# Performance work log

Hardware: AMD Instinct MI355X
Metric: run time of the kernel (lower is better)

Reference implementation:

```python
import jax, jax.numpy as jnp
import numpy as np

D_MODEL = 1024
D_STATE = 16
D_CONV = 4
D_INNER = 2 * D_MODEL          # expand * d_model
DT_RANK = (D_MODEL + 15) // 16 # ceil(d_model/16) = 64
BATCH, SEQLEN = 2, 1024


def setup_inputs() -> dict:
    key = jax.random.key(0)
    ks = jax.random.split(key, 8)
    s = lambda k, shape, scale=0.02: (jax.random.normal(k, shape, jnp.float32) * scale)
    return {
        "hidden_states": jax.random.normal(ks[0], (BATCH, SEQLEN, D_MODEL), jnp.float32),
        "in_proj_w": s(ks[1], (2 * D_INNER, D_MODEL)),
        "conv_w": s(ks[2], (D_INNER, 1, D_CONV), 0.3),   # depthwise conv kernel (O, I/groups=1, K)
        "conv_b": jnp.zeros((D_INNER,), jnp.float32),
        "x_proj_w": s(ks[3], (DT_RANK + 2 * D_STATE, D_INNER)),
        "dt_proj_w": s(ks[4], (D_INNER, DT_RANK), 0.1),
        # inverse-softplus of small dt values, like the torch init
        "dt_proj_b": jax.random.uniform(ks[5], (D_INNER,), jnp.float32, minval=-5.0, maxval=-2.0),
        "A_log": jnp.log(jnp.broadcast_to(jnp.arange(1, D_STATE + 1, dtype=jnp.float32), (D_INNER, D_STATE))),
        "D": jnp.ones((D_INNER,), jnp.float32),
        "out_proj_w": s(ks[6], (D_MODEL, D_INNER)),
    }


def _forward(hidden_states, in_proj_w, conv_w, conv_b, x_proj_w,
             dt_proj_w, dt_proj_b, A_log, D, out_proj_w):
    B, L, _ = hidden_states.shape
    # in_proj -> split into x, z
    xz = hidden_states @ in_proj_w.T                      # [B, L, 2*d_inner]
    x, z = jnp.split(xz, 2, axis=-1)
    # causal depthwise conv1d (pad left d_conv-1, then take first L) + SiLU
    xc = jnp.transpose(x, (0, 2, 1))                      # [B, d_inner, L]
    xc = jax.lax.conv_general_dilated(
        xc, conv_w, window_strides=(1,), padding=[(D_CONV - 1, 0)],
        feature_group_count=D_INNER,
        dimension_numbers=("NCH", "OIH", "NCH")) + conv_b[None, :, None]
    xc = jax.nn.silu(xc)
    u = jnp.transpose(xc, (0, 2, 1)).astype(jnp.float32)  # [B, L, d_inner]
    # x_proj -> dt_low, B, C
    x_dbl = u @ x_proj_w.T                                # [B, L, dt_rank + 2*d_state]
    dt_low, Bp, Cp = jnp.split(x_dbl, [DT_RANK, DT_RANK + D_STATE], axis=-1)
    dt = dt_low @ dt_proj_w.T + dt_proj_b                 # [B, L, d_inner]
    # NOTE: original adds dt_proj.bias AGAIN as delta_bias inside the scan, then softplus
    delta = jax.nn.softplus(dt + dt_proj_b)
    A = -jnp.exp(A_log.astype(jnp.float32))               # [d_inner, d_state]
    # discretization
    dA = jnp.exp(jnp.einsum("bld,dn->lbdn", delta, A))    # [L, B, d, n]
    dBu = jnp.einsum("bld,bln,bld->lbdn", delta, Bp.astype(jnp.float32), u)
    C_t = jnp.transpose(Cp.astype(jnp.float32), (1, 0, 2))  # [L, B, n]

    def step(state, inp):
        a, b, c = inp
        state = a * state + b                             # [B, d, n]
        y = jnp.einsum("bdn,bn->bd", state, c)
        return state, y

    x0 = jnp.zeros((B, D_INNER, D_STATE), jnp.float32)
    _, ys = jax.lax.scan(step, x0, (dA, dBu, C_t))        # ys: [L, B, d]
    y = jnp.transpose(ys, (1, 0, 2))                      # [B, L, d]
    y = y + u * D.astype(jnp.float32)                     # skip connection
    y = y * jax.nn.silu(z.astype(jnp.float32))            # gating
    y = y.astype(hidden_states.dtype)
    return y @ out_proj_w.T                               # [B, L, d_model]


def reference(hidden_states, in_proj_w, conv_w, conv_b, x_proj_w,
              dt_proj_w, dt_proj_b, A_log, D, out_proj_w):
    return _forward(hidden_states, in_proj_w, conv_w, conv_b, x_proj_w,
                    dt_proj_w, dt_proj_b, A_log, D, out_proj_w)
```

## Files before the change

kernel.cpp:

```cpp
#include <hip/hip_runtime.h>
#include <hip/hip_bf16.h>
#include <math.h>

#define BATCH   2
#define SEQLEN  1024
#define DMODEL  1024
#define DINNER  2048
#define DSTATE  16
#define DTRANK  64
#define XPAD    128
#define MROWS   (BATCH*SEQLEN)
#define NSEG2   32
#define SEGL2   (SEQLEN/NSEG2)
#define XP_SPLIT  8
#define OUT_SPLIT 2

typedef float    f32x4  __attribute__((ext_vector_type(4)));
typedef _Float16 f16x8  __attribute__((ext_vector_type(8)));
typedef _Float16 f16x4  __attribute__((ext_vector_type(4)));

template<int EPI>
__global__ __launch_bounds__(256) void pgemm64(
    const _Float16* __restrict__ A, int lda,
    const _Float16* __restrict__ W, int ldw,
    float* __restrict__ C, int ldc, int K,
    const float* __restrict__ bias, _Float16* __restrict__ C16, size_t zstride)
{
  constexpr int APS = 520;
  constexpr int BPS = 1032;
  __shared__ _Float16 As[2][8 * APS];
  __shared__ _Float16 Bs[2][8 * BPS];

  const int t  = threadIdx.x;
  const int m0 = blockIdx.y * 64, n0 = blockIdx.x * 128;
  const int kchunk = K / gridDim.z;
  const int kbeg = blockIdx.z * kchunk;
  const int nIter = kchunk / 64;

  const int kb = t & 7;
  const int r0 = t >> 3;
  const _Float16* gA = A + (size_t)(m0 + r0) * lda + kbeg + kb * 8;
  const _Float16* gB = W + (size_t)(n0 + r0) * ldw + kbeg + kb * 8;
  const size_t a32 = (size_t)32 * lda;
  const size_t b32 = (size_t)32 * ldw;
  const int aoff = kb * APS + r0 * 8;
  const int boff = kb * BPS + r0 * 8;

  {
    f16x8 a0 = *(const f16x8*)(gA);
    f16x8 a1 = *(const f16x8*)(gA + a32);
    f16x8 b0 = *(const f16x8*)(gB);
    f16x8 b1 = *(const f16x8*)(gB + b32);
    f16x8 b2 = *(const f16x8*)(gB + 2 * b32);
    f16x8 b3 = *(const f16x8*)(gB + 3 * b32);
    gA += 64; gB += 64;
    *(f16x8*)&As[0][aoff]       = a0;
    *(f16x8*)&As[0][aoff + 256] = a1;
    *(f16x8*)&Bs[0][boff]       = b0;
    *(f16x8*)&Bs[0][boff + 256] = b1;
    *(f16x8*)&Bs[0][boff + 512] = b2;
    *(f16x8*)&Bs[0][boff + 768] = b3;
  }

  const int lane = t & 63, wvi = t >> 6;
  const int wn = wvi * 32;
  const int lm = lane & 15, lk = lane >> 4;

  f32x4 acc[4][2] = {};

  for (int it = 0; it < nIter; ++it) {
    __syncthreads();
    const bool more = (it + 1 < nIter);
    f16x8 a0, a1, b0, b1, b2, b3;
    if (more) {
      a0 = *(const f16x8*)(gA);
      a1 = *(const f16x8*)(gA + a32);
      b0 = *(const f16x8*)(gB);
      b1 = *(const f16x8*)(gB + b32);
      b2 = *(const f16x8*)(gB + 2 * b32);
      b3 = *(const f16x8*)(gB + 3 * b32);
      gA += 64; gB += 64;
    }
    const int cb = it & 1;
#pragma unroll
    for (int s = 0; s < 2; ++s) {
      f16x8 av[4], bv[2];
#pragma unroll
      for (int i = 0; i < 4; ++i)
        av[i] = *(const f16x8*)&As[cb][(s * 4 + lk) * APS + (i * 16 + lm) * 8];
#pragma unroll
      for (int j = 0; j < 2; ++j)
        bv[j] = *(const f16x8*)&Bs[cb][(s * 4 + lk) * BPS + (wn + j * 16 + lm) * 8];
#pragma unroll
      for (int i = 0; i < 4; ++i)
#pragma unroll
        for (int j = 0; j < 2; ++j)
          acc[i][j] = __builtin_amdgcn_mfma_f32_16x16x32_f16(av[i], bv[j], acc[i][j], 0, 0, 0);
    }
    if (more) {
      const int nb = (it + 1) & 1;
      *(f16x8*)&As[nb][aoff]       = a0;
      *(f16x8*)&As[nb][aoff + 256] = a1;
      *(f16x8*)&Bs[nb][boff]       = b0;
      *(f16x8*)&Bs[nb][boff + 256] = b1;
      *(f16x8*)&Bs[nb][boff + 512] = b2;
      *(f16x8*)&Bs[nb][boff + 768] = b3;
    }
  }

  float* Cz = C + (size_t)blockIdx.z * zstride;
#pragma unroll
  for (int i = 0; i < 4; ++i) {
    const int mrow = m0 + i * 16 + lk * 4;
#pragma unroll
    for (int j = 0; j < 2; ++j) {
      const int col = n0 + wn + j * 16 + lm;
#pragma unroll
      for (int r = 0; r < 4; ++r)
        Cz[(size_t)(mrow + r) * ldc + col] = acc[i][j][r];
    }
  }
}

template<int EPI>
__global__ __launch_bounds__(256) void pgemm128(
    const _Float16* __restrict__ A, int lda,
    const _Float16* __restrict__ W, int ldw,
    float* __restrict__ C, int ldc, int K,
    _Float16* __restrict__ C16, size_t zstride)
{
  constexpr int PS = 1032;
  __shared__ _Float16 As[2][8 * PS];
  __shared__ _Float16 Bs[2][8 * PS];

  const int t  = threadIdx.x;
  const int m0 = blockIdx.y * 128, n0 = blockIdx.x * 128;
  const int kchunk = K / gridDim.z;
  const int kbeg = blockIdx.z * kchunk;
  const int nIter = kchunk / 64;

  const int kb = t & 7;
  const int r0 = t >> 3;
  const _Float16* gA = A + (size_t)(m0 + r0) * lda + kbeg + kb * 8;
  const _Float16* gB = W + (size_t)(n0 + r0) * ldw + kbeg + kb * 8;
  const size_t a32 = (size_t)32 * lda;
  const size_t b32 = (size_t)32 * ldw;
  const int soff = kb * PS + r0 * 8;

  {
    f16x8 ar[4], br[4];
#pragma unroll
    for (int j = 0; j < 4; ++j) {
      ar[j] = *(const f16x8*)(gA + j * a32);
      br[j] = *(const f16x8*)(gB + j * b32);
    }
    gA += 64; gB += 64;
#pragma unroll
    for (int j = 0; j < 4; ++j) {
      *(f16x8*)&As[0][soff + j * 256] = ar[j];
      *(f16x8*)&Bs[0][soff + j * 256] = br[j];
    }
  }

  const int lane = t & 63, wvi = t >> 6;
  const int wm = (wvi >> 1) * 64, wn = (wvi & 1) * 64;
  const int lm = lane & 15, lk = lane >> 4;

  f32x4 acc[4][4] = {};

  for (int it = 0; it < nIter; ++it) {
    __syncthreads();
    const bool more = (it + 1 < nIter);
    f16x8 ar[4], br[4];
    if (more) {
#pragma unroll
      for (int j = 0; j < 4; ++j) {
        ar[j] = *(const f16x8*)(gA + j * a32);
        br[j] = *(const f16x8*)(gB + j * b32);
      }
      gA += 64; gB += 64;
    }
    const int cb = it & 1;
#pragma unroll
    for (int s = 0; s < 2; ++s) {
      f16x8 av[4], bv[4];
#pragma unroll
      for (int i = 0; i < 4; ++i)
        av[i] = *(const f16x8*)&As[cb][(s * 4 + lk) * PS + (wm + i * 16 + lm) * 8];
#pragma unroll
      for (int j = 0; j < 4; ++j)
        bv[j] = *(const f16x8*)&Bs[cb][(s * 4 + lk) * PS + (wn + j * 16 + lm) * 8];
#pragma unroll
      for (int i = 0; i < 4; ++i)
#pragma unroll
        for (int j = 0; j < 4; ++j)
          acc[i][j] = __builtin_amdgcn_mfma_f32_16x16x32_f16(av[i], bv[j], acc[i][j], 0, 0, 0);
    }
    if (more) {
      const int nb = (it + 1) & 1;
#pragma unroll
      for (int j = 0; j < 4; ++j) {
        *(f16x8*)&As[nb][soff + j * 256] = ar[j];
        *(f16x8*)&Bs[nb][soff + j * 256] = br[j];
      }
    }
  }

  float* Cz = C + (size_t)blockIdx.z * zstride;
#pragma unroll
  for (int i = 0; i < 4; ++i) {
    const int mrow = m0 + wm + i * 16 + lk * 4;
#pragma unroll
    for (int j = 0; j < 4; ++j) {
      const int col = n0 + wn + j * 16 + lm;
#pragma unroll
      for (int r = 0; r < 4; ++r) {
        float v = acc[i][j][r];
        size_t off = (size_t)(mrow + r) * ldc + col;
        if constexpr (EPI == 0) {
          Cz[off] = v;
        } else {
          C16[off] = (_Float16)v;
        }
      }
    }
  }
}

#define R0 (MROWS * DMODEL / 4)
#define R1 (2 * DINNER * DMODEL / 4)
#define R2 (DMODEL * DINNER / 4)
#define R4 (XPAD * DINNER / 4)
#define F2H_TOTAL (R0 + R1 + R2 + R4)

__global__ __launch_bounds__(256) void f2h_all(
    const float* __restrict__ hid, const float* __restrict__ w_in,
    const float* __restrict__ w_out, const float* __restrict__ w_xp,
    _Float16* __restrict__ hid16, _Float16* __restrict__ w_in16,
    _Float16* __restrict__ w_out16, _Float16* __restrict__ w_xp16)
{
  int i = blockIdx.x * 256 + threadIdx.x;
  const float* src; _Float16* dst; int off;
  if (i < R0)                     { src = hid;   dst = hid16;   off = i; }
  else if (i < R0+R1)             { src = w_in;  dst = w_in16;  off = i - R0; }
  else if (i < R0+R1+R2)          { src = w_out; dst = w_out16; off = i - (R0+R1); }
  else if (i < F2H_TOTAL) {
    off = i - (R0+R1+R2);
    int r = (off * 4) >> 11;
    f16x4 h = {0, 0, 0, 0};
    if (r < 96) {
      float4 v = ((const float4*)w_xp)[off];
      h = (f16x4){(_Float16)v.x, (_Float16)v.y, (_Float16)v.z, (_Float16)v.w};
    }
    ((f16x4*)w_xp16)[off] = h;
    return;
  } else return;
  float4 v = ((const float4*)src)[off];
  ((f16x4*)dst)[off] = (f16x4){(_Float16)v.x, (_Float16)v.y, (_Float16)v.z, (_Float16)v.w};
}

__global__ __launch_bounds__(256) void reduce_xdbl(
    const float* __restrict__ part,
    float* __restrict__ xdbl32)
{
  int i = blockIdx.x * 256 + threadIdx.x;
  f32x4 s = ((const f32x4*)part)[i];
#pragma unroll
  for (int z = 1; z < XP_SPLIT; ++z)
    s += ((const f32x4*)part)[(size_t)z * (MROWS * XPAD / 4) + i];
  ((f32x4*)xdbl32)[i] = s;
}

__global__ __launch_bounds__(256) void reduce_out(
    const float* __restrict__ part, float* __restrict__ out)
{
  int i = blockIdx.x * 256 + threadIdx.x;
  f32x4 s = ((const f32x4*)part)[i];
#pragma unroll
  for (int z = 1; z < OUT_SPLIT; ++z)
    s += ((const f32x4*)part)[(size_t)z * (MROWS * DMODEL / 4) + i];
  ((f32x4*)out)[i] = s;
}

__global__ __launch_bounds__(256) void conv_silu(
    const _Float16* __restrict__ xz16,
    const float* __restrict__ conv_w,
    const float* __restrict__ conv_b,
    _Float16* __restrict__ u16)
{
  const int idx = blockIdx.x * 256 + threadIdx.x;
  const int d   = idx & (DINNER - 1);
  const int row = idx >> 11;
  const int l   = row & (SEQLEN - 1);
  float s = conv_b[d];
#pragma unroll
  for (int k = 0; k < 4; ++k) {
    int lt = l + k - 3;
    if (lt >= 0)
      s = fmaf((float)xz16[(size_t)(row + k - 3) * (2 * DINNER) + d],
               conv_w[d * 4 + k], s);
  }
  float v = s / (1.f + __expf(-s));
  u16[idx] = (_Float16)v;
}

__global__ __launch_bounds__(256) void scan_pe(
    const _Float16* __restrict__ u16,
    const float* __restrict__ x_dbl,
    const float* __restrict__ A_log,
    const float* __restrict__ dt_w,
    const float* __restrict__ dt_b,
    float* __restrict__ pbuf, float* __restrict__ ebuf,
    _Float16* __restrict__ delta16)
{
  const int t = threadIdx.x;
  const int d = blockIdx.x * 256 + t;
  const int b   = blockIdx.y >> 5;
  const int seg = blockIdx.y & 31;
  const int row0 = b * SEQLEN + seg * SEGL2;

  f32x4 w[16];
#pragma unroll
  for (int q = 0; q < 16; ++q)
    w[q] = *(const f32x4*)&dt_w[(size_t)d * DTRANK + q * 4];
  const float b2 = 2.f * dt_b[d];

  float A_dn[DSTATE];
#pragma unroll
  for (int q = 0; q < 4; ++q) {
    f32x4 a4 = *(const f32x4*)&A_log[(size_t)d * DSTATE + q * 4];
#pragma unroll
    for (int e = 0; e < 4; ++e) A_dn[q * 4 + e] = -__expf(a4[e]);
  }

  __shared__ __align__(16) float xd[SEGL2 * 64];
  __shared__ __align__(16) float Bl[SEGL2 * DSTATE];
  {
#pragma unroll
    for (int k = 0; k < 2; ++k) {
      int idx = t * 2 + k;
      int i = idx >> 4, c4 = (idx & 15) * 4;
      *(f32x4*)&xd[i * 64 + c4] =
          *(const f32x4*)&x_dbl[(size_t)(row0 + i) * XPAD + c4];
    }
    if (t < 128) {
      int i = t >> 2, n4 = (t & 3) * 4;
      *(f32x4*)&Bl[i * DSTATE + n4] =
          *(const f32x4*)&x_dbl[(size_t)(row0 + i) * XPAD + DTRANK + n4];
    }
  }
  __syncthreads();

  float E[DSTATE];
#pragma unroll
  for (int n = 0; n < DSTATE; ++n) E[n] = 0.f;
  float S = 0.f;

  for (int i = 0; i < SEGL2; ++i) {
    float a = b2;
#pragma unroll
    for (int q = 0; q < 16; ++q) {
      f32x4 x4 = *(const f32x4*)&xd[i * 64 + q * 4];
      a = fmaf(x4[0], w[q][0], a);
      a = fmaf(x4[1], w[q][1], a);
      a = fmaf(x4[2], w[q][2], a);
      a = fmaf(x4[3], w[q][3], a);
    }
    float dv = (a > 20.f) ? a : __logf(1.f + __expf(a));
    const size_t ro = (size_t)(row0 + i) * DINNER + d;
    delta16[ro] = (_Float16)dv;
    dv = (float)(_Float16)dv;
    float uv = (float)u16[ro];
    float du = dv * uv;
    S += dv;
#pragma unroll
    for (int n = 0; n < DSTATE; ++n) {
      float dA = __expf(dv * A_dn[n]);
      E[n] = fmaf(dA, E[n], du * Bl[i * DSTATE + n]);
    }
  }

  const size_t base = ((size_t)(b * NSEG2 + seg) * DSTATE) * DINNER + d;
#pragma unroll
  for (int n = 0; n < DSTATE; ++n) {
    pbuf[base + (size_t)n * DINNER] = __expf(S * A_dn[n]);
    ebuf[base + (size_t)n * DINNER] = E[n];
  }
}

__global__ __launch_bounds__(256) void scan_mid(
    const float* __restrict__ pbuf, const float* __restrict__ ebuf,
    float* __restrict__ cbuf)
{
  const int idx = blockIdx.x * 256 + threadIdx.x;
  const int d = idx & (DINNER - 1);
  const int n = (idx >> 11) & 15;
  const int b = idx >> 15;
  float s = 0.f;
  for (int seg = 0; seg < NSEG2; ++seg) {
    const size_t off = ((size_t)(b * NSEG2 + seg) * DSTATE + n) * DINNER + d;
    cbuf[off] = s;
    s = fmaf(pbuf[off], s, ebuf[off]);
  }
}

__global__ __launch_bounds__(256) void scan_y(
    const _Float16* __restrict__ delta16,
    const _Float16* __restrict__ u16,
    const _Float16* __restrict__ xz16,
    const float* __restrict__ x_dbl,
    const float* __restrict__ A_log,
    const float* __restrict__ Dp,
    const float* __restrict__ cbuf,
    _Float16* __restrict__ y16)
{
  const int t = threadIdx.x;
  const int d = blockIdx.x * 256 + t;
  const int b   = blockIdx.y >> 5;
  const int seg = blockIdx.y & 31;
  const int row0 = b * SEQLEN + seg * SEGL2;

  float A_dn[DSTATE];
#pragma unroll
  for (int q = 0; q < 4; ++q) {
    f32x4 a4 = *(const f32x4*)&A_log[(size_t)d * DSTATE + q * 4];
#pragma unroll
    for (int e = 0; e < 4; ++e) A_dn[q * 4 + e] = -__expf(a4[e]);
  }
  const float Dv = Dp[d];

  __shared__ __align__(16) float Bl[SEGL2 * DSTATE];
  __shared__ __align__(16) float Cl[SEGL2 * DSTATE];
  if (t < 128) {
    int i = t >> 2, n4 = (t & 3) * 4;
    *(f32x4*)&Bl[i * DSTATE + n4] =
        *(const f32x4*)&x_dbl[(size_t)(row0 + i) * XPAD + DTRANK + n4];
  } else {
    int u = t - 128;
    int i = u >> 2, n4 = (u & 3) * 4;
    *(f32x4*)&Cl[i * DSTATE + n4] =
        *(const f32x4*)&x_dbl[(size_t)(row0 + i) * XPAD + DTRANK + DSTATE + n4];
  }
  __syncthreads();

  float s[DSTATE];
  {
    const size_t base = ((size_t)(b * NSEG2 + seg) * DSTATE) * DINNER + d;
#pragma unroll
    for (int n = 0; n < DSTATE; ++n) s[n] = cbuf[base + (size_t)n * DINNER];
  }

  for (int i = 0; i < SEGL2; ++i) {
    const size_t ro = (size_t)(row0 + i) * DINNER + d;
    float dv = (float)delta16[ro];
    float uv = (float)u16[ro];
    float zv = (float)xz16[(size_t)(row0 + i) * (2 * DINNER) + DINNER + d];
    float du = dv * uv;
    float y = 0.f;
#pragma unroll
    for (int n = 0; n < DSTATE; ++n) {
      float dA = __expf(dv * A_dn[n]);
      s[n] = fmaf(dA, s[n], du * Bl[i * DSTATE + n]);
      y = fmaf(s[n], Cl[i * DSTATE + n], y);
    }
    y = fmaf(uv, Dv, y);
    y *= zv / (1.f + __expf(-zv));
    y16[ro] = (_Float16)y;
  }
}

extern "C" void kernel_launch(void* const* d_in, const int* in_sizes, int n_in,
                              void* d_out, int out_size, void* d_ws, size_t ws_size,
                              hipStream_t stream)
{
  const float* hidden     = (const float*)d_in[0];
  const float* in_proj_w  = (const float*)d_in[1];
  const float* conv_w     = (const float*)d_in[2];
  const float* conv_b     = (const float*)d_in[3];
  const float* x_proj_w   = (const float*)d_in[4];
  const float* dt_proj_w  = (const float*)d_in[5];
  const float* dt_proj_b  = (const float*)d_in[6];
  const float* A_log      = (const float*)d_in[7];
  const float* Dp         = (const float*)d_in[8];
  const float* out_proj_w = (const float*)d_in[9];
  float* out = (float*)d_out;

  char* p = (char*)d_ws;
  _Float16* xz16    = (_Float16*)p;  p += (size_t)MROWS * 2 * DINNER * 2;
  _Float16* u16     = (_Float16*)p;  p += (size_t)MROWS * DINNER * 2;
  float*    xdbl32  = (float*)p;     p += (size_t)MROWS * XPAD * 4;
  _Float16* delta16 = (_Float16*)p;  p += (size_t)MROWS * DINNER * 2;
  _Float16* h16     = (_Float16*)p;  p += (size_t)MROWS * DMODEL * 2;
  _Float16* win16   = (_Float16*)p;  p += (size_t)2 * DINNER * DMODEL * 2;
  _Float16* wout16  = (_Float16*)p;  p += (size_t)DMODEL * DINNER * 2;
  _Float16* wxp16   = (_Float16*)p;  p += (size_t)XPAD * DINNER * 2;
  _Float16* y16     = (_Float16*)p;  p += (size_t)MROWS * DINNER * 2;
  float*    pbuf    = (float*)p;     p += (size_t)BATCH * NSEG2 * DSTATE * DINNER * 4;
  float*    ebuf    = (float*)p;     p += (size_t)BATCH * NSEG2 * DSTATE * DINNER * 4;
  float*    cbuf    = (float*)p;     p += (size_t)BATCH * NSEG2 * DSTATE * DINNER * 4;
  float*    xp_part  = (float*)delta16;
  float*    out_part = (float*)xz16;

  f2h_all<<<(F2H_TOTAL + 255) / 256, 256, 0, stream>>>(
      hidden, in_proj_w, out_proj_w, x_proj_w,
      h16, win16, wout16, wxp16);

  pgemm128<4><<<dim3(4096 / 128, MROWS / 128, 1), 256, 0, stream>>>(
      h16, DMODEL, win16, DMODEL, nullptr, 4096, DMODEL, xz16, 0);

  conv_silu<<<(MROWS * DINNER) / 256, 256, 0, stream>>>(xz16, conv_w, conv_b, u16);

  pgemm64<0><<<dim3(1, MROWS / 64, XP_SPLIT), 256, 0, stream>>>(
      u16, DINNER, wxp16, DINNER, xp_part, XPAD, DINNER, nullptr, nullptr,
      (size_t)MROWS * XPAD);

  reduce_xdbl<<<(MROWS * XPAD / 4) / 256, 256, 0, stream>>>(xp_part, xdbl32);

  scan_pe<<<dim3(DINNER / 256, BATCH * NSEG2), 256, 0, stream>>>(
      u16, xdbl32, A_log, dt_proj_w, dt_proj_b, pbuf, ebuf, delta16);
  scan_mid<<<(BATCH * DSTATE * DINNER) / 256, 256, 0, stream>>>(pbuf, ebuf, cbuf);
  scan_y<<<dim3(DINNER / 256, BATCH * NSEG2), 256, 0, stream>>>(
      delta16, u16, xz16, xdbl32, A_log, Dp, cbuf, y16);

  pgemm128<0><<<dim3(DMODEL / 128, MROWS / 128, OUT_SPLIT), 256, 0, stream>>>(
      y16, DINNER, wout16, DINNER, out_part, DMODEL, DINNER, nullptr,
      (size_t)MROWS * DMODEL);

  reduce_out<<<(MROWS * DMODEL / 4) / 256, 256, 0, stream>>>(out_part, out);
}
```

Measured before the change: 230.8 us.

## Fuse fp32-to-fp16 conversion into GEMM loads and drop split-K reduce kernels

Removes the standalone f2h_all conversion kernel: the GEMMs now load fp32 activations and weights and convert them to fp16 in registers before staging them in LDS. The x_proj split-K partial sums are reduced on the fly inside scan_pe and scan_y instead of in a separate reduce kernel. The out_proj GEMM now uses a 64-row tile with no K split and writes fp32 output directly, which removes the reduce_out kernel. This saves three launches and the fp16 copy traffic, but the GEMMs read twice the bytes for converted operands, and the scan kernels now do eight reads per x_dbl element.

```diff
diff --git a/kernel.cpp b/kernel.cpp
--- a/kernel.cpp
+++ b/kernel.cpp
@@ -13,18 +13,120 @@
 #define NSEG2   32
 #define SEGL2   (SEQLEN/NSEG2)
 #define XP_SPLIT  8
-#define OUT_SPLIT 2
 
 typedef float    f32x4  __attribute__((ext_vector_type(4)));
 typedef _Float16 f16x8  __attribute__((ext_vector_type(8)));
 typedef _Float16 f16x4  __attribute__((ext_vector_type(4)));
 
-template<int EPI>
-__global__ __launch_bounds__(256) void pgemm64(
+__device__ __forceinline__ f16x8 cvt_f32x8(const float* p) {
+  float4 a = *(const float4*)p;
+  float4 b = *(const float4*)(p + 4);
+  f16x8 r;
+  r[0] = (_Float16)a.x; r[1] = (_Float16)a.y;
+  r[2] = (_Float16)a.z; r[3] = (_Float16)a.w;
+  r[4] = (_Float16)b.x; r[5] = (_Float16)b.y;
+  r[6] = (_Float16)b.z; r[7] = (_Float16)b.w;
+  return r;
+}
+
+__global__ __launch_bounds__(256) void pgemm128_f32(
+    const float* __restrict__ A, int lda,
+    const float* __restrict__ W, int ldw,
+    _Float16* __restrict__ C16, int ldc, int K)
+{
+  constexpr int PS = 1032;
+  __shared__ _Float16 As[2][8 * PS];
+  __shared__ _Float16 Bs[2][8 * PS];
+
+  const int t  = threadIdx.x;
+  const int m0 = blockIdx.y * 128, n0 = blockIdx.x * 128;
+  const int nIter = K / 64;
+
+  const int kb = t & 7;
+  const int r0 = t >> 3;
+  const float* gA = A + (size_t)(m0 + r0) * lda + kb * 8;
+  const float* gB = W + (size_t)(n0 + r0) * ldw + kb * 8;
+  const size_t a32 = (size_t)32 * lda;
+  const size_t b32 = (size_t)32 * ldw;
+  const int soff = kb * PS + r0 * 8;
+
+  {
+    f16x8 ar[4], br[4];
+#pragma unroll
+    for (int j = 0; j < 4; ++j) {
+      ar[j] = cvt_f32x8(gA + j * a32);
+      br[j] = cvt_f32x8(gB + j * b32);
+    }
+    gA += 64; gB += 64;
+#pragma unroll
+    for (int j = 0; j < 4; ++j) {
+      *(f16x8*)&As[0][soff + j * 256] = ar[j];
+      *(f16x8*)&Bs[0][soff + j * 256] = br[j];
+    }
+  }
+
+  const int lane = t & 63, wvi = t >> 6;
+  const int wm = (wvi >> 1) * 64, wn = (wvi & 1) * 64;
+  const int lm = lane & 15, lk = lane >> 4;
+
+  f32x4 acc[4][4] = {};
+
+  for (int it = 0; it < nIter; ++it) {
+    __syncthreads();
+    const bool more = (it + 1 < nIter);
+    f16x8 ar[4], br[4];
+    if (more) {
+#pragma unroll
+      for (int j = 0; j < 4; ++j) {
+        ar[j] = cvt_f32x8(gA + j * a32);
+        br[j] = cvt_f32x8(gB + j * b32);
+      }
+      gA += 64; gB += 64;
+    }
+    const int cb = it & 1;
+#pragma unroll
+    for (int s = 0; s < 2; ++s) {
+      f16x8 av[4], bv[4];
+#pragma unroll
+      for (int i = 0; i < 4; ++i)
+        av[i] = *(const f16x8*)&As[cb][(s * 4 + lk) * PS + (wm + i * 16 + lm) * 8];
+#pragma unroll
+      for (int j = 0; j < 4; ++j)
+        bv[j] = *(const f16x8*)&Bs[cb][(s * 4 + lk) * PS + (wn + j * 16 + lm) * 8];
+#pragma unroll
+      for (int i = 0; i < 4; ++i)
+#pragma unroll
+        for (int j = 0; j < 4; ++j)
+          acc[i][j] = __builtin_amdgcn_mfma_f32_16x16x32_f16(av[i], bv[j], acc[i][j], 0, 0, 0);
+    }
+    if (more) {
+      const int nb = (it + 1) & 1;
+#pragma unroll
+      for (int j = 0; j < 4; ++j) {
+        *(f16x8*)&As[nb][soff + j * 256] = ar[j];
+        *(f16x8*)&Bs[nb][soff + j * 256] = br[j];
+      }
+    }
+  }
+
+#pragma unroll
+  for (int i = 0; i < 4; ++i) {
+    const int mrow = m0 + wm + i * 16 + lk * 4;
+#pragma unroll
+    for (int j = 0; j < 4; ++j) {
+      const int col = n0 + wn + j * 16 + lm;
+#pragma unroll
+      for (int r = 0; r < 4; ++r)
+        C16[(size_t)(mrow + r) * ldc + col] = (_Float16)acc[i][j][r];
+    }
+  }
+}
+
+template<int WROWS>
+__global__ __launch_bounds__(256) void pgemm64f(
     const _Float16* __restrict__ A, int lda,
-    const _Float16* __restrict__ W, int ldw,
-    float* __restrict__ C, int ldc, int K,
-    const float* __restrict__ bias, _Float16* __restrict__ C16, size_t zstride)
+    const float* __restrict__ Wf, int ldw,
+    float* __restrict__ C, int ldc, int K, size_t zstride)
 {
   constexpr int APS = 520;
   constexpr int BPS = 1032;
@@ -40,7 +142,7 @@
   const int kb = t & 7;
   const int r0 = t >> 3;
   const _Float16* gA = A + (size_t)(m0 + r0) * lda + kbeg + kb * 8;
-  const _Float16* gB = W + (size_t)(n0 + r0) * ldw + kbeg + kb * 8;
+  const float*    gB = Wf + (size_t)(n0 + r0) * ldw + kbeg + kb * 8;
   const size_t a32 = (size_t)32 * lda;
   const size_t b32 = (size_t)32 * ldw;
   const int aoff = kb * APS + r0 * 8;
@@ -49,17 +151,18 @@
   {
     f16x8 a0 = *(const f16x8*)(gA);
     f16x8 a1 = *(const f16x8*)(gA + a32);
-    f16x8 b0 = *(const f16x8*)(gB);
-    f16x8 b1 = *(const f16x8*)(gB + b32);
-    f16x8 b2 = *(const f16x8*)(gB + 2 * b32);
-    f16x8 b3 = *(const f16x8*)(gB + 3 * b32);
+    f16x8 br[4];
+#pragma unroll
+    for (int j = 0; j < 4; ++j) {
+      if (n0 + r0 + 32 * j < WROWS) br[j] = cvt_f32x8(gB + j * b32);
+      else                          br[j] = (f16x8){};
+    }
     gA += 64; gB += 64;
     *(f16x8*)&As[0][aoff]       = a0;
     *(f16x8*)&As[0][aoff + 256] = a1;
-    *(f16x8*)&Bs[0][boff]       = b0;
-    *(f16x8*)&Bs[0][boff + 256] = b1;
-    *(f16x8*)&Bs[0][boff + 512] = b2;
-    *(f16x8*)&Bs[0][boff + 768] = b3;
+#pragma unroll
+    for (int j = 0; j < 4; ++j)
+      *(f16x8*)&Bs[0][boff + j * 256] = br[j];
   }
 
   const int lane = t & 63, wvi = t >> 6;
@@ -71,14 +174,15 @@
   for (int it = 0; it < nIter; ++it) {
     __syncthreads();
     const bool more = (it + 1 < nIter);
-    f16x8 a0, a1, b0, b1, b2, b3;
+    f16x8 a0, a1, br[4];
     if (more) {
       a0 = *(const f16x8*)(gA);
       a1 = *(const f16x8*)(gA + a32);
-      b0 = *(const f16x8*)(gB);
-      b1 = *(const f16x8*)(gB + b32);
-      b2 = *(const f16x8*)(gB + 2 * b32);
-      b3 = *(const f16x8*)(gB + 3 * b32);
+#pragma unroll
+      for (int j = 0; j < 4; ++j) {
+        if (n0 + r0 + 32 * j < WROWS) br[j] = cvt_f32x8(gB + j * b32);
+        else                          br[j] = (f16x8){};
+      }
       gA += 64; gB += 64;
     }
     const int cb = it & 1;
@@ -101,10 +205,9 @@
       const int nb = (it + 1) & 1;
       *(f16x8*)&As[nb][aoff]       = a0;
       *(f16x8*)&As[nb][aoff + 256] = a1;
-      *(f16x8*)&Bs[nb][boff]       = b0;
-      *(f16x8*)&Bs[nb][boff + 256] = b1;
-      *(f16x8*)&Bs[nb][boff + 512] = b2;
-      *(f16x8*)&Bs[nb][boff + 768] = b3;
+#pragma unroll
+      for (int j = 0; j < 4; ++j)
+        *(f16x8*)&Bs[nb][boff + j * 256] = br[j];
     }
   }
 
@@ -120,166 +223,6 @@
         Cz[(size_t)(mrow + r) * ldc + col] = acc[i][j][r];
     }
   }
-}
-
-template<int EPI>
-__global__ __launch_bounds__(256) void pgemm128(
-    const _Float16* __restrict__ A, int lda,
-    const _Float16* __restrict__ W, int ldw,
-    float* __restrict__ C, int ldc, int K,
-    _Float16* __restrict__ C16, size_t zstride)
-{
-  constexpr int PS = 1032;
-  __shared__ _Float16 As[2][8 * PS];
-  __shared__ _Float16 Bs[2][8 * PS];
-
-  const int t  = threadIdx.x;
-  const int m0 = blockIdx.y * 128, n0 = blockIdx.x * 128;
-  const int kchunk = K / gridDim.z;
-  const int kbeg = blockIdx.z * kchunk;
-  const int nIter = kchunk / 64;
-
-  const int kb = t & 7;
-  const int r0 = t >> 3;
-  const _Float16* gA = A + (size_t)(m0 + r0) * lda + kbeg + kb * 8;
-  const _Float16* gB = W + (size_t)(n0 + r0) * ldw + kbeg + kb * 8;
-  const size_t a32 = (size_t)32 * lda;
-  const size_t b32 = (size_t)32 * ldw;
-  const int soff = kb * PS + r0 * 8;
-
-  {
-    f16x8 ar[4], br[4];
-#pragma unroll
-    for (int j = 0; j < 4; ++j) {
-      ar[j] = *(const f16x8*)(gA + j * a32);
-      br[j] = *(const f16x8*)(gB + j * b32);
-    }
-    gA += 64; gB += 64;
-#pragma unroll
-    for (int j = 0; j < 4; ++j) {
-      *(f16x8*)&As[0][soff + j * 256] = ar[j];
-      *(f16x8*)&Bs[0][soff + j * 256] = br[j];
-    }
-  }
-
-  const int lane = t & 63, wvi = t >> 6;
-  const int wm = (wvi >> 1) * 64, wn = (wvi & 1) * 64;
-  const int lm = lane & 15, lk = lane >> 4;
-
-  f32x4 acc[4][4] = {};
-
-  for (int it = 0; it < nIter; ++it) {
-    __syncthreads();
-    const bool more = (it + 1 < nIter);
-    f16x8 ar[4], br[4];
-    if (more) {
-#pragma unroll
-      for (int j = 0; j < 4; ++j) {
-        ar[j] = *(const f16x8*)(gA + j * a32);
-        br[j] = *(const f16x8*)(gB + j * b32);
-      }
-      gA += 64; gB += 64;
-    }
-    const int cb = it & 1;
-#pragma unroll
-    for (int s = 0; s < 2; ++s) {
-      f16x8 av[4], bv[4];
-#pragma unroll
-      for (int i = 0; i < 4; ++i)
-        av[i] = *(const f16x8*)&As[cb][(s * 4 + lk) * PS + (wm + i * 16 + lm) * 8];
-#pragma unroll
-      for (int j = 0; j < 4; ++j)
-        bv[j] = *(const f16x8*)&Bs[cb][(s * 4 + lk) * PS + (wn + j * 16 + lm) * 8];
-#pragma unroll
-      for (int i = 0; i < 4; ++i)
-#pragma unroll
-        for (int j = 0; j < 4; ++j)
-          acc[i][j] = __builtin_amdgcn_mfma_f32_16x16x32_f16(av[i], bv[j], acc[i][j], 0, 0, 0);
-    }
-    if (more) {
-      const int nb = (it + 1) & 1;
-#pragma unroll
-      for (int j = 0; j < 4; ++j) {
-        *(f16x8*)&As[nb][soff + j * 256] = ar[j];
-        *(f16x8*)&Bs[nb][soff + j * 256] = br[j];
-      }
-    }
-  }
-
-  float* Cz = C + (size_t)blockIdx.z * zstride;
-#pragma unroll
-  for (int i = 0; i < 4; ++i) {
-    const int mrow = m0 + wm + i * 16 + lk * 4;
-#pragma unroll
-    for (int j = 0; j < 4; ++j) {
-      const int col = n0 + wn + j * 16 + lm;
-#pragma unroll
-      for (int r = 0; r < 4; ++r) {
-        float v = acc[i][j][r];
-        size_t off = (size_t)(mrow + r) * ldc + col;
-        if constexpr (EPI == 0) {
-          Cz[off] = v;
-        } else {
-          C16[off] = (_Float16)v;
-        }
-      }
-    }
-  }
-}
-
-#define R0 (MROWS * DMODEL / 4)
-#define R1 (2 * DINNER * DMODEL / 4)
-#define R2 (DMODEL * DINNER / 4)
-#define R4 (XPAD * DINNER / 4)
-#define F2H_TOTAL (R0 + R1 + R2 + R4)
-
-__global__ __launch_bounds__(256) void f2h_all(
-    const float* __restrict__ hid, const float* __restrict__ w_in,
-    const float* __restrict__ w_out, const float* __restrict__ w_xp,
-    _Float16* __restrict__ hid16, _Float16* __restrict__ w_in16,
-    _Float16* __restrict__ w_out16, _Float16* __restrict__ w_xp16)
-{
-  int i = blockIdx.x * 256 + threadIdx.x;
-  const float* src; _Float16* dst; int off;
-  if (i < R0)                     { src = hid;   dst = hid16;   off = i; }
-  else if (i < R0+R1)             { src = w_in;  dst = w_in16;  off = i - R0; }
-  else if (i < R0+R1+R2)          { src = w_out; dst = w_out16; off = i - (R0+R1); }
-  else if (i < F2H_TOTAL) {
-    off = i - (R0+R1+R2);
-    int r = (off * 4) >> 11;
-    f16x4 h = {0, 0, 0, 0};
-    if (r < 96) {
-      float4 v = ((const float4*)w_xp)[off];
-      h = (f16x4){(_Float16)v.x, (_Float16)v.y, (_Float16)v.z, (_Float16)v.w};
-    }
-    ((f16x4*)w_xp16)[off] = h;
-    return;
-  } else return;
-  float4 v = ((const float4*)src)[off];
-  ((f16x4*)dst)[off] = (f16x4){(_Float16)v.x, (_Float16)v.y, (_Float16)v.z, (_Float16)v.w};
-}
-
-__global__ __launch_bounds__(256) void reduce_xdbl(
-    const float* __restrict__ part,
-    float* __restrict__ xdbl32)
-{
-  int i = blockIdx.x * 256 + threadIdx.x;
-  f32x4 s = ((const f32x4*)part)[i];
-#pragma unroll
-  for (int z = 1; z < XP_SPLIT; ++z)
-    s += ((const f32x4*)part)[(size_t)z * (MROWS * XPAD / 4) + i];
-  ((f32x4*)xdbl32)[i] = s;
-}
-
-__global__ __launch_bounds__(256) void reduce_out(
-    const float* __restrict__ part, float* __restrict__ out)
-{
-  int i = blockIdx.x * 256 + threadIdx.x;
-  f32x4 s = ((const f32x4*)part)[i];
-#pragma unroll
-  for (int z = 1; z < OUT_SPLIT; ++z)
-    s += ((const f32x4*)part)[(size_t)z * (MROWS * DMODEL / 4) + i];
-  ((f32x4*)out)[i] = s;
 }
 
 __global__ __launch_bounds__(256) void conv_silu(
@@ -304,9 +247,17 @@
   u16[idx] = (_Float16)v;
 }
 
+__device__ __forceinline__ f32x4 red8(const float* __restrict__ part, size_t idx) {
+  f32x4 s = *(const f32x4*)(part + idx);
+#pragma unroll
+  for (int z = 1; z < XP_SPLIT; ++z)
+    s += *(const f32x4*)(part + (size_t)z * (MROWS * XPAD) + idx);
+  return s;
+}
+
 __global__ __launch_bounds__(256) void scan_pe(
     const _Float16* __restrict__ u16,
-    const float* __restrict__ x_dbl,
+    const float* __restrict__ part,
     const float* __restrict__ A_log,
     const float* __restrict__ dt_w,
     const float* __restrict__ dt_b,
@@ -340,13 +291,12 @@
     for (int k = 0; k < 2; ++k) {
       int idx = t * 2 + k;
       int i = idx >> 4, c4 = (idx & 15) * 4;
-      *(f32x4*)&xd[i * 64 + c4] =
-          *(const f32x4*)&x_dbl[(size_t)(row0 + i) * XPAD + c4];
+      *(f32x4*)&xd[i * 64 + c4] = red8(part, (size_t)(row0 + i) * XPAD + c4);
     }
     if (t < 128) {
       int i = t >> 2, n4 = (t & 3) * 4;
       *(f32x4*)&Bl[i * DSTATE + n4] =
-          *(const f32x4*)&x_dbl[(size_t)(row0 + i) * XPAD + DTRANK + n4];
+          red8(part, (size_t)(row0 + i) * XPAD + DTRANK + n4);
     }
   }
   __syncthreads();
@@ -408,7 +358,7 @@
     const _Float16* __restrict__ delta16,
     const _Float16* __restrict__ u16,
     const _Float16* __restrict__ xz16,
-    const float* __restrict__ x_dbl,
+    const float* __restrict__ part,
     const float* __restrict__ A_log,
     const float* __restrict__ Dp,
     const float* __restrict__ cbuf,
@@ -434,12 +384,12 @@
   if (t < 128) {
     int i = t >> 2, n4 = (t & 3) * 4;
     *(f32x4*)&Bl[i * DSTATE + n4] =
-        *(const f32x4*)&x_dbl[(size_t)(row0 + i) * XPAD + DTRANK + n4];
+        red8(part, (size_t)(row0 + i) * XPAD + DTRANK + n4);
   } else {
     int u = t - 128;
     int i = u >> 2, n4 = (u & 3) * 4;
     *(f32x4*)&Cl[i * DSTATE + n4] =
-        *(const f32x4*)&x_dbl[(size_t)(row0 + i) * XPAD + DTRANK + DSTATE + n4];
+        red8(part, (size_t)(row0 + i) * XPAD + DTRANK + DSTATE + n4);
   }
   __syncthreads();
 
@@ -488,43 +438,28 @@
   char* p = (char*)d_ws;
   _Float16* xz16    = (_Float16*)p;  p += (size_t)MROWS * 2 * DINNER * 2;
   _Float16* u16     = (_Float16*)p;  p += (size_t)MROWS * DINNER * 2;
-  float*    xdbl32  = (float*)p;     p += (size_t)MROWS * XPAD * 4;
   _Float16* delta16 = (_Float16*)p;  p += (size_t)MROWS * DINNER * 2;
-  _Float16* h16     = (_Float16*)p;  p += (size_t)MROWS * DMODEL * 2;
-  _Float16* win16   = (_Float16*)p;  p += (size_t)2 * DINNER * DMODEL * 2;
-  _Float16* wout16  = (_Float16*)p;  p += (size_t)DMODEL * DINNER * 2;
-  _Float16* wxp16   = (_Float16*)p;  p += (size_t)XPAD * DINNER * 2;
   _Float16* y16     = (_Float16*)p;  p += (size_t)MROWS * DINNER * 2;
+  float*    xp_part = (float*)p;     p += (size_t)XP_SPLIT * MROWS * XPAD * 4;
   float*    pbuf    = (float*)p;     p += (size_t)BATCH * NSEG2 * DSTATE * DINNER * 4;
   float*    ebuf    = (float*)p;     p += (size_t)BATCH * NSEG2 * DSTATE * DINNER * 4;
   float*    cbuf    = (float*)p;     p += (size_t)BATCH * NSEG2 * DSTATE * DINNER * 4;
-  float*    xp_part  = (float*)delta16;
-  float*    out_part = (float*)xz16;
-
-  f2h_all<<<(F2H_TOTAL + 255) / 256, 256, 0, stream>>>(
-      hidden, in_proj_w, out_proj_w, x_proj_w,
-      h16, win16, wout16, wxp16);
-
-  pgemm128<4><<<dim3(4096 / 128, MROWS / 128, 1), 256, 0, stream>>>(
-      h16, DMODEL, win16, DMODEL, nullptr, 4096, DMODEL, xz16, 0);
+
+  pgemm128_f32<<<dim3(4096 / 128, MROWS / 128), 256, 0, stream>>>(
+      hidden, DMODEL, in_proj_w, DMODEL, xz16, 4096, DMODEL);
 
   conv_silu<<<(MROWS * DINNER) / 256, 256, 0, stream>>>(xz16, conv_w, conv_b, u16);
 
-  pgemm64<0><<<dim3(1, MROWS / 64, XP_SPLIT), 256, 0, stream>>>(
-      u16, DINNER, wxp16, DINNER, xp_part, XPAD, DINNER, nullptr, nullptr,
+  pgemm64f<96><<<dim3(1, MROWS / 64, XP_SPLIT), 256, 0, stream>>>(
+      u16, DINNER, x_proj_w, DINNER, xp_part, XPAD, DINNER,
       (size_t)MROWS * XPAD);
 
-  reduce_xdbl<<<(MROWS * XPAD / 4) / 256, 256, 0, stream>>>(xp_part, xdbl32);
-
   scan_pe<<<dim3(DINNER / 256, BATCH * NSEG2), 256, 0, stream>>>(
-      u16, xdbl32, A_log, dt_proj_w, dt_proj_b, pbuf, ebuf, delta16);
+      u16, xp_part, A_log, dt_proj_w, dt_proj_b, pbuf, ebuf, delta16);
   scan_mid<<<(BATCH * DSTATE * DINNER) / 256, 256, 0, stream>>>(pbuf, ebuf, cbuf);
   scan_y<<<dim3(DINNER / 256, BATCH * NSEG2), 256, 0, stream>>>(
-      delta16, u16, xz16, xdbl32, A_log, Dp, cbuf, y16);
-
-  pgemm128<0><<<dim3(DMODEL / 128, MROWS / 128, OUT_SPLIT), 256, 0, stream>>>(
-      y16, DINNER, wout16, DINNER, out_part, DMODEL, DINNER, nullptr,
-      (size_t)MROWS * DMODEL);
-
-  reduce_out<<<(MROWS * DMODEL / 4) / 256, 256, 0, stream>>>(out_part, out);
-}
+      delta16, u16, xz16, xp_part, A_log, Dp, cbuf, y16);
+
+  pgemm64f<DMODEL><<<dim3(DMODEL / 128, MROWS / 64, 1), 256, 0, stream>>>(
+      y16, DINNER, out_proj_w, DINNER, out, DMODEL, DINNER, 0);
+}
```

Result: slower. 287.4 us (+24.5%).
